# Kernel optimization log

Hardware: AMD Instinct MI355X
Metric: run time of the kernel (lower is better)

## Reference

```python
import jax, jax.numpy as jnp
import numpy as np


def _three_nn(parent_xyz, xyz):
    # parent_xyz: (bs, n, 3) queries; xyz: (bs, m, 3) reference points.
    # Squared pairwise distances (bs, n, m) without forming (x-y)^2 tensor of rank 4.
    d2 = (jnp.sum(parent_xyz**2, -1, keepdims=True)
          - 2.0 * jnp.einsum('bnd,bmd->bnm', parent_xyz, xyz)
          + jnp.sum(xyz**2, -1)[:, None, :])
    neg_d2, idx = jax.lax.top_k(-d2, 3)           # 3 smallest distances
    dist = jnp.sqrt(jnp.maximum(-neg_d2, 0.0))    # pointnet2 returns sqrt(dist2)
    return dist, idx                              # (bs, n, 3), (bs, n, 3)


def _three_interpolate(feats, idx, weight):
    # feats: (bs, c, m); idx, weight: (bs, n, 3) -> (bs, c, n)
    feats_t = jnp.swapaxes(feats, 1, 2)                     # (bs, m, c)
    gathered = jax.vmap(lambda f, i: f[i])(feats_t, idx)    # (bs, n, 3, c)
    out = jnp.einsum('bnkc,bnk->bcn', gathered, weight)
    return out


def _conv1x1(x, W, b):
    # x: (bs, c_in, n); W: (c_out, c_in); b: (c_out,)
    return jnp.einsum('oc,bcn->bon', W, x) + b[None, :, None]


def setup_inputs() -> dict:
    key = jax.random.key(0)
    ks = jax.random.split(key, 6)
    bs, m, n = 8, 1024, 4096
    c0, c1, c2 = 256, 128, 256
    xyz = jax.random.normal(ks[0], (bs, m, 3), jnp.float32)
    parent_xyz = jax.random.normal(ks[1], (bs, n, 3), jnp.float32)
    feats = jax.random.normal(ks[2], (bs, c0, m), jnp.float32)
    skip_feats = jax.random.normal(ks[3], (bs, c1, n), jnp.float32)
    W1 = jax.random.normal(ks[4], (c2, c0 + c1), jnp.float32) * (1.0 / np.sqrt(c0 + c1))
    b1 = jnp.zeros((c2,), jnp.float32)
    W2 = jax.random.normal(ks[5], (c2, c2), jnp.float32) * (1.0 / np.sqrt(c2))
    b2 = jnp.zeros((c2,), jnp.float32)
    return {"xyz": xyz, "parent_xyz": parent_xyz, "feats": feats,
            "skip_feats": skip_feats, "W1": W1, "b1": b1, "W2": W2, "b2": b2}


def reference(xyz, parent_xyz, feats, skip_feats, W1, b1, W2, b2):
    dist, idx = _three_nn(parent_xyz, xyz)
    inv_dist = 1.0 / (dist + 1e-8)
    weight = inv_dist / jnp.sum(inv_dist, 2, keepdims=True)     # (bs, n, 3)
    up_feats = _three_interpolate(feats, idx, weight)           # (bs, c0, n)
    parent_feats = jnp.concatenate([up_feats, skip_feats], 1)   # (bs, c0+c1, n)
    h = jax.nn.relu(_conv1x1(parent_feats, W1, b1))
    out = jax.nn.relu(_conv1x1(h, W2, b2))
    return out
```

## Files before the change

kernel.cpp:

```cpp
#include <hip/hip_runtime.h>
#include <hip/hip_bf16.h>
#include <cstddef>
#include <cstdint>

#define BS    8
#define M_PTS 1024
#define N_PTS 4096
#define C0    256
#define C1    128
#define C2    256
#define K1DIM 384

typedef __attribute__((ext_vector_type(8))) short bf16x8;
typedef __attribute__((ext_vector_type(4))) float f32x4;

__device__ __forceinline__ ushort f2bf(float f) {
  union { float f; unsigned u; } v; v.f = f;
  unsigned r = v.u + 0x7fffu + ((v.u >> 16) & 1u);
  return (ushort)(r >> 16);
}
__device__ __forceinline__ ushort bf16c(float f) {
  return __builtin_bit_cast(ushort, __float2bfloat16(f));
}

__device__ __forceinline__ float rdlane_f(float v, int lane) {
  union { float f; int i; } u; u.f = v;
  u.i = __builtin_amdgcn_readlane(u.i, lane);
  return u.f;
}

__global__ __launch_bounds__(256) void prep_k(
    const float* __restrict__ feats, const float* __restrict__ W1,
    const float* __restrict__ W2, float* __restrict__ featsT,
    ushort* __restrict__ W1f, ushort* __restrict__ W2f) {
  __shared__ float tile[32][33];
  const int t = threadIdx.x;
  if (blockIdx.x < 2048) {
    const int bx = blockIdx.x & 31;
    const int by = (blockIdx.x >> 5) & 7;
    const int bz = blockIdx.x >> 8;
    const int tx = t & 31, ty = t >> 5;
    const float* ip = feats + (size_t)bz * C0 * M_PTS;
    float*       op = featsT + (size_t)bz * C0 * M_PTS;
    const int r0 = by * 32, c0 = bx * 32;
#pragma unroll
    for (int i = 0; i < 4; ++i)
      tile[ty + i * 8][tx] = ip[(size_t)(r0 + ty + i * 8) * M_PTS + c0 + tx];
    __syncthreads();
#pragma unroll
    for (int i = 0; i < 4; ++i)
      op[(size_t)(c0 + ty + i * 8) * C0 + r0 + tx] = tile[tx][ty + i * 8];
  } else {
    const int id = (blockIdx.x - 2048) * 256 + t;
    if (id < C2 * K1DIM) {
      int m = id / K1DIM, k = id - m * K1DIM;
      int off = (((m >> 4) * 12 + (k >> 5)) * 4 + ((k >> 3) & 3)) * 128 + (m & 15) * 8 + (k & 7);
      W1f[off] = f2bf(W1[id]);
    }
    if (id < C2 * C2) {
      int m = id >> 8, k = id & 255;
      int off = (((m >> 4) * 8 + (k >> 5)) * 4 + ((k >> 3) & 3)) * 128 + (m & 15) * 8 + (k & 7);
      W2f[off] = f2bf(W2[id]);
    }
  }
}

__global__ __launch_bounds__(256, 4) void fp_fused_k(
    const float* __restrict__ xyz,
    const float* __restrict__ pxyz,
    const float* __restrict__ featsT,
    const float* __restrict__ skip,
    const ushort* __restrict__ W1f,
    const float* __restrict__ b1,
    const ushort* __restrict__ W2f,
    const float* __restrict__ b2,
    float* __restrict__ out) {
  __shared__ float4 smemq[2560];
  float4* pts4 = smemq;
  ushort* pfB  = (ushort*)(smemq + 1024);
  ushort* hbuf = (ushort*)smemq;

  const int t  = threadIdx.x;
  const int b  = blockIdx.x & 7;
  const int n0 = (blockIdx.x >> 3) * 32;
  const int wv = t >> 6, l = t & 63;
  const int q  = t >> 3, sub = t & 7;

  const float qx = pxyz[((size_t)b * N_PTS + n0 + q) * 3 + 0];
  const float qy = pxyz[((size_t)b * N_PTS + n0 + q) * 3 + 1];
  const float qz = pxyz[((size_t)b * N_PTS + n0 + q) * 3 + 2];

#pragma unroll
  for (int it = 0; it < 2; ++it) {
    const int p = t + it * 256;
    const float2* xb = (const float2*)(xyz + (size_t)b * 3 * M_PTS + 6 * p);
    const float2 A = xb[0], B = xb[1], C = xb[2];
    const float x0 = A.x, y0 = A.y, z0 = B.x, x1 = B.y, y1 = C.x, z1 = C.y;
    const float s0 = __fadd_rn(__fadd_rn(__fmul_rn(x0, x0), __fmul_rn(y0, y0)),
                               __fmul_rn(z0, z0));
    const float s1 = __fadd_rn(__fadd_rn(__fmul_rn(x1, x1), __fmul_rn(y1, y1)),
                               __fmul_rn(z1, z1));
    const int U = p ^ ((p >> 6) & 7);
    pts4[U * 2 + 0] = (float4){x0 + x0, x1 + x1, y0 + y0, y1 + y1};
    pts4[U * 2 + 1] = (float4){z0 + z0, z1 + z1, s0, s1};
  }

  float skp[16];
#pragma unroll
  for (int it = 0; it < 8; ++it) {
    const int id = t + it * 256;
    const int r2 = id >> 5, nn = id & 31;
    skp[2 * it + 0] = skip[((size_t)b * C1 + 2 * r2 + 0) * N_PTS + n0 + nn];
    skp[2 * it + 1] = skip[((size_t)b * C1 + 2 * r2 + 1) * N_PTS + n0 + nn];
  }

  const float qq = __fadd_rn(__fadd_rn(__fmul_rn(qx, qx), __fmul_rn(qy, qy)),
                             __fmul_rn(qz, qz));
  __syncthreads();

  float d0 = 3.4e38f, d1 = 3.4e38f, d2 = 3.4e38f;
  int   i0 = 0, i1 = 0, i2 = 0;
  {
    int pe[8];
#pragma unroll
    for (int e = 0; e < 8; ++e) pe[e] = (sub * 64 + (e ^ sub)) * 2;
    for (int jb = 0; jb < 8; ++jb) {
#pragma unroll
      for (int e = 0; e < 8; ++e) {
        const float4 A  = pts4[pe[e] + jb * 16];
        const float4 Bv = pts4[pe[e] + jb * 16 + 1];
        {
          const float dot2 = __fadd_rn(__fadd_rn(__fmul_rn(qx, A.x), __fmul_rn(qy, A.z)),
                                       __fmul_rn(qz, Bv.x));
          const float d = __fadd_rn(__fsub_rn(qq, dot2), Bv.z);
          const int m = jb * 16 + 2 * e;
          const bool c0 = d < d0, c1 = d < d1, c2 = d < d2;
          i2 = c1 ? i1 : (c2 ? m : i2);
          i1 = c0 ? i0 : (c1 ? m : i1);
          i0 = c0 ? m : i0;
          d2 = __builtin_amdgcn_fmed3f(d, d1, d2);
          d1 = __builtin_amdgcn_fmed3f(d, d0, d1);
          d0 = fminf(d, d0);
        }
        {
          const float dot2 = __fadd_rn(__fadd_rn(__fmul_rn(qx, A.y), __fmul_rn(qy, A.w)),
                                       __fmul_rn(qz, Bv.y));
          const float d = __fadd_rn(__fsub_rn(qq, dot2), Bv.w);
          const int m = jb * 16 + 2 * e + 1;
          const bool c0 = d < d0, c1 = d < d1, c2 = d < d2;
          i2 = c1 ? i1 : (c2 ? m : i2);
          i1 = c0 ? i0 : (c1 ? m : i1);
          i0 = c0 ? m : i0;
          d2 = __builtin_amdgcn_fmed3f(d, d1, d2);
          d1 = __builtin_amdgcn_fmed3f(d, d0, d1);
          d0 = fminf(d, d0);
        }
      }
    }
    i0 += sub * 128; i1 += sub * 128; i2 += sub * 128;
  }

#pragma unroll
  for (int mk = 1; mk <= 4; mk <<= 1) {
    const float pd0 = __shfl_xor(d0, mk), pd1 = __shfl_xor(d1, mk), pd2 = __shfl_xor(d2, mk);
    const int   pi0 = __shfl_xor(i0, mk), pi1 = __shfl_xor(i1, mk), pi2 = __shfl_xor(i2, mk);
    const bool lo = (sub & mk) == 0;
    const float a0 = lo ? d0 : pd0, a1 = lo ? d1 : pd1, a2 = lo ? d2 : pd2;
    const float b0 = lo ? pd0 : d0, b1v = lo ? pd1 : d1, b2v = lo ? pd2 : d2;
    const int   A0 = lo ? i0 : pi0, A1 = lo ? i1 : pi1, A2 = lo ? i2 : pi2;
    const int   B0 = lo ? pi0 : i0, B1 = lo ? pi1 : i1, B2 = lo ? pi2 : i2;
    const bool c0 = b0 < a0;
    const bool cb1a0 = b1v < a0, cb0a1 = b0 < a1;
    const bool cb1a1 = b1v < a1, cb2a0 = b2v < a0, cb0a2 = b0 < a2;
    const float m0 = c0 ? b0 : a0;                 const int M0 = c0 ? B0 : A0;
    const float t1a = cb1a0 ? b1v : a0;            const int T1a = cb1a0 ? B1 : A0;
    const float t1b = cb0a1 ? b0 : a1;             const int T1b = cb0a1 ? B0 : A1;
    const float m1 = c0 ? t1a : t1b;               const int M1 = c0 ? T1a : T1b;
    const float sA = cb2a0 ? b2v : a0;             const int SA = cb2a0 ? B2 : A0;
    const float sB = cb1a1 ? b1v : a1;             const int SB = cb1a1 ? B1 : A1;
    const float sD = cb0a2 ? b0 : a2;              const int SD = cb0a2 ? B0 : A2;
    const float m2 = c0 ? (cb1a0 ? sA : sB) : (cb0a1 ? sB : sD);
    const int   M2 = c0 ? (cb1a0 ? SA : SB) : (cb0a1 ? SB : SD);
    d0 = m0; d1 = m1; d2 = m2; i0 = M0; i1 = M1; i2 = M2;
  }

  float w0f, w1f, w2f;
  {
    const float t0 = sqrtf(fmaxf(d0, 0.f)), t1 = sqrtf(fmaxf(d1, 0.f)),
                t2 = sqrtf(fmaxf(d2, 0.f));
    const float r0 = 1.0f / (t0 + 1e-8f), r1 = 1.0f / (t1 + 1e-8f),
                r2 = 1.0f / (t2 + 1e-8f);
    const float rs = __fadd_rn(__fadd_rn(r0, r1), r2);
    w0f = r0 / rs; w1f = r1 / rs; w2f = r2 / rs;
  }

  {
    const float* fb = featsT + (size_t)b * M_PTS * C0;
    float cw0 = rdlane_f(w0f, 0), cw1 = rdlane_f(w1f, 0), cw2 = rdlane_f(w2f, 0);
    float4 cf0 = *(const float4*)(fb + (size_t)__builtin_amdgcn_readlane(i0, 0) * C0 + l * 4);
    float4 cf1 = *(const float4*)(fb + (size_t)__builtin_amdgcn_readlane(i1, 0) * C0 + l * 4);
    float4 cf2 = *(const float4*)(fb + (size_t)__builtin_amdgcn_readlane(i2, 0) * C0 + l * 4);
#pragma unroll
    for (int qi = 0; qi < 8; ++qi) {
      float nw0, nw1, nw2; float4 nf0, nf1, nf2;
      if (qi < 7) {
        const int src = (qi + 1) * 8;
        nw0 = rdlane_f(w0f, src); nw1 = rdlane_f(w1f, src); nw2 = rdlane_f(w2f, src);
        nf0 = *(const float4*)(fb + (size_t)__builtin_amdgcn_readlane(i0, src) * C0 + l * 4);
        nf1 = *(const float4*)(fb + (size_t)__builtin_amdgcn_readlane(i1, src) * C0 + l * 4);
        nf2 = *(const float4*)(fb + (size_t)__builtin_amdgcn_readlane(i2, src) * C0 + l * 4);
      }
      ushort4 hv;
      hv.x = bf16c(cw0 * cf0.x + cw1 * cf1.x + cw2 * cf2.x);
      hv.y = bf16c(cw0 * cf0.y + cw1 * cf1.y + cw2 * cf2.y);
      hv.z = bf16c(cw0 * cf0.z + cw1 * cf1.z + cw2 * cf2.z);
      hv.w = bf16c(cw0 * cf0.w + cw1 * cf1.w + cw2 * cf2.w);
      const int nq = wv * 8 + qi;
      const int kq = l >> 1;
      const int u = kq * 32 + (nq ^ (kq & 7));
      *reinterpret_cast<ushort4*>(&pfB[u * 8 + (l & 1) * 4]) = hv;
      if (qi < 7) { cf0 = nf0; cf1 = nf1; cf2 = nf2; cw0 = nw0; cw1 = nw1; cw2 = nw2; }
    }
  }
#pragma unroll
  for (int it = 0; it < 8; ++it) {
    const int id = t + it * 256;
    const int r2 = id >> 5, nn = id & 31;
    const int k = C0 + 2 * r2;
    const int kq = k >> 3;
    const int u = kq * 32 + (nn ^ (kq & 7));
    ushort2 sv; sv.x = bf16c(skp[2 * it]); sv.y = bf16c(skp[2 * it + 1]);
    *reinterpret_cast<ushort2*>(&pfB[u * 8 + (k & 7)]) = sv;
  }
  __syncthreads();

  const int c = l & 15, g = l >> 4;

  f32x4 acc[4][2];
#pragma unroll
  for (int i = 0; i < 4; ++i)
#pragma unroll
    for (int j = 0; j < 2; ++j) acc[i][j] = (f32x4){0.f, 0.f, 0.f, 0.f};

  {
    bf16x8 afr[4], nafr[4];
#pragma unroll
    for (int i = 0; i < 4; ++i)
      afr[i] = *reinterpret_cast<const bf16x8*>(&W1f[(((wv * 4 + i) * 12 + 0) * 4 + g) * 128 + c * 8]);
    for (int kb = 0; kb < 12; ++kb) {
      const int kqg = kb * 4 + g;
      bf16x8 bfr[2];
#pragma unroll
      for (int j = 0; j < 2; ++j)
        bfr[j] = *reinterpret_cast<const bf16x8*>(&pfB[(kqg * 32 + ((j * 16 + c) ^ (kqg & 7))) * 8]);
      if (kb < 11) {
#pragma unroll
        for (int i = 0; i < 4; ++i)
          nafr[i] = *reinterpret_cast<const bf16x8*>(&W1f[(((wv * 4 + i) * 12 + kb + 1) * 4 + g) * 128 + c * 8]);
      }
      __builtin_amdgcn_s_setprio(1);
#pragma unroll
      for (int i = 0; i < 4; ++i)
#pragma unroll
        for (int j = 0; j < 2; ++j)
          acc[i][j] = __builtin_amdgcn_mfma_f32_16x16x32_bf16(afr[i], bfr[j], acc[i][j], 0, 0, 0);
      __builtin_amdgcn_s_setprio(0);
      if (kb < 11) {
#pragma unroll
        for (int i = 0; i < 4; ++i) afr[i] = nafr[i];
      }
    }
  }

#pragma unroll
  for (int i = 0; i < 4; ++i) {
    const int mbase = wv * 64 + i * 16 + g * 4;
    const float4 bias = *(const float4*)(b1 + mbase);
#pragma unroll
    for (int j = 0; j < 2; ++j) {
      const int nn = j * 16 + c;
      const int kq = mbase >> 3;
      const int u = kq * 32 + (nn ^ (kq & 7));
      ushort4 hv;
      hv.x = bf16c(fmaxf(acc[i][j].x + bias.x, 0.f));
      hv.y = bf16c(fmaxf(acc[i][j].y + bias.y, 0.f));
      hv.z = bf16c(fmaxf(acc[i][j].z + bias.z, 0.f));
      hv.w = bf16c(fmaxf(acc[i][j].w + bias.w, 0.f));
      *reinterpret_cast<ushort4*>(&hbuf[u * 8 + (mbase & 7)]) = hv;
    }
  }
  __syncthreads();

#pragma unroll
  for (int i = 0; i < 4; ++i)
#pragma unroll
    for (int j = 0; j < 2; ++j) acc[i][j] = (f32x4){0.f, 0.f, 0.f, 0.f};

  {
    bf16x8 afr[4], nafr[4];
#pragma unroll
    for (int i = 0; i < 4; ++i)
      afr[i] = *reinterpret_cast<const bf16x8*>(&W2f[(((wv * 4 + i) * 8 + 0) * 4 + g) * 128 + c * 8]);
    for (int kb = 0; kb < 8; ++kb) {
      const int kqg = kb * 4 + g;
      bf16x8 bfr[2];
#pragma unroll
      for (int j = 0; j < 2; ++j)
        bfr[j] = *reinterpret_cast<const bf16x8*>(&hbuf[(kqg * 32 + ((j * 16 + c) ^ (kqg & 7))) * 8]);
      if (kb < 7) {
#pragma unroll
        for (int i = 0; i < 4; ++i)
          nafr[i] = *reinterpret_cast<const bf16x8*>(&W2f[(((wv * 4 + i) * 8 + kb + 1) * 4 + g) * 128 + c * 8]);
      }
      __builtin_amdgcn_s_setprio(1);
#pragma unroll
      for (int i = 0; i < 4; ++i)
#pragma unroll
        for (int j = 0; j < 2; ++j)
          acc[i][j] = __builtin_amdgcn_mfma_f32_16x16x32_bf16(afr[i], bfr[j], acc[i][j], 0, 0, 0);
      __builtin_amdgcn_s_setprio(0);
      if (kb < 7) {
#pragma unroll
        for (int i = 0; i < 4; ++i) afr[i] = nafr[i];
      }
    }
  }

#pragma unroll
  for (int i = 0; i < 4; ++i) {
    const int mbase = wv * 64 + i * 16 + g * 4;
    const float4 bias = *(const float4*)(b2 + mbase);
#pragma unroll
    for (int j = 0; j < 2; ++j) {
      const int nn = n0 + j * 16 + c;
      out[((size_t)b * C2 + mbase + 0) * N_PTS + nn] = fmaxf(acc[i][j].x + bias.x, 0.f);
      out[((size_t)b * C2 + mbase + 1) * N_PTS + nn] = fmaxf(acc[i][j].y + bias.y, 0.f);
      out[((size_t)b * C2 + mbase + 2) * N_PTS + nn] = fmaxf(acc[i][j].z + bias.z, 0.f);
      out[((size_t)b * C2 + mbase + 3) * N_PTS + nn] = fmaxf(acc[i][j].w + bias.w, 0.f);
    }
  }
}

extern "C" void kernel_launch(void* const* d_in, const int* in_sizes, int n_in,
                              void* d_out, int out_size, void* d_ws, size_t ws_size,
                              hipStream_t stream) {
  const float* xyz   = (const float*)d_in[0];
  const float* pxyz  = (const float*)d_in[1];
  const float* feats = (const float*)d_in[2];
  const float* skip  = (const float*)d_in[3];
  const float* W1    = (const float*)d_in[4];
  const float* b1    = (const float*)d_in[5];
  const float* W2    = (const float*)d_in[6];
  const float* b2    = (const float*)d_in[7];
  float* out = (float*)d_out;

  float*  ws     = (float*)d_ws;
  float*  featsT = ws;
  ushort* W1f    = (ushort*)(featsT + (size_t)BS * M_PTS * C0);
  ushort* W2f    = W1f + (size_t)C2 * K1DIM;

  prep_k<<<2432, 256, 0, stream>>>(feats, W1, W2, featsT, W1f, W2f);
  fp_fused_k<<<BS * (N_PTS / 32), 256, 0, stream>>>(xyz, pxyz, featsT, skip,
                                                    W1f, b1, W2f, b2, out);
}
```

Measured before the change: 45.55 us.

## Precompute W1·feats at coarse points and interpolate projected features

Uses linearity of the interpolation and the first 1x1 conv: the prep kernel now computes G = W1[:, :C0]·feats at the m coarse points with MFMA and stores it transposed. The fused kernel then interpolates G rows straight into the accumulators. The first GEMM shrinks to only the skip-feature K range (128 instead of 384), and the per-query gather of 256-channel feature rows is replaced by gathers of 256-wide projected rows. This trades a feats transpose for a small extra GEMM over m=1024 points. It also changes rounding, since the interpolation now runs in fp32 on bf16-projected results instead of bf16-rounding the interpolated features.

```diff
diff --git a/kernel.cpp b/kernel.cpp
--- a/kernel.cpp
+++ b/kernel.cpp
@@ -23,35 +23,13 @@
   return __builtin_bit_cast(ushort, __float2bfloat16(f));
 }
 
-__device__ __forceinline__ float rdlane_f(float v, int lane) {
-  union { float f; int i; } u; u.f = v;
-  u.i = __builtin_amdgcn_readlane(u.i, lane);
-  return u.f;
-}
-
 __global__ __launch_bounds__(256) void prep_k(
     const float* __restrict__ feats, const float* __restrict__ W1,
-    const float* __restrict__ W2, float* __restrict__ featsT,
-    ushort* __restrict__ W1f, ushort* __restrict__ W2f) {
-  __shared__ float tile[32][33];
+    const float* __restrict__ W2, ushort* __restrict__ W1f,
+    ushort* __restrict__ W2f, float* __restrict__ Gt) {
   const int t = threadIdx.x;
-  if (blockIdx.x < 2048) {
-    const int bx = blockIdx.x & 31;
-    const int by = (blockIdx.x >> 5) & 7;
-    const int bz = blockIdx.x >> 8;
-    const int tx = t & 31, ty = t >> 5;
-    const float* ip = feats + (size_t)bz * C0 * M_PTS;
-    float*       op = featsT + (size_t)bz * C0 * M_PTS;
-    const int r0 = by * 32, c0 = bx * 32;
-#pragma unroll
-    for (int i = 0; i < 4; ++i)
-      tile[ty + i * 8][tx] = ip[(size_t)(r0 + ty + i * 8) * M_PTS + c0 + tx];
-    __syncthreads();
-#pragma unroll
-    for (int i = 0; i < 4; ++i)
-      op[(size_t)(c0 + ty + i * 8) * C0 + r0 + tx] = tile[tx][ty + i * 8];
-  } else {
-    const int id = (blockIdx.x - 2048) * 256 + t;
+  if (blockIdx.x < 384) {
+    const int id = blockIdx.x * 256 + t;
     if (id < C2 * K1DIM) {
       int m = id / K1DIM, k = id - m * K1DIM;
       int off = (((m >> 4) * 12 + (k >> 5)) * 4 + ((k >> 3) & 3)) * 128 + (m & 15) * 8 + (k & 7);
@@ -62,23 +40,84 @@
       int off = (((m >> 4) * 8 + (k >> 5)) * 4 + ((k >> 3) & 3)) * 128 + (m & 15) * 8 + (k & 7);
       W2f[off] = f2bf(W2[id]);
     }
-  }
+    return;
+  }
+  __shared__ ushort Bt[16384];
+  const int id2 = blockIdx.x - 384;
+  const int bz = id2 & 7;
+  const int m0 = (id2 >> 3) * 64;
+  const float* fb = feats + (size_t)bz * C0 * M_PTS;
+
+#pragma unroll
+  for (int it = 0; it < 16; ++it) {
+    const int cc = it * 16 + (t >> 4);
+    const int nl = (t & 15) * 4;
+    const float4 v = *(const float4*)(fb + (size_t)cc * M_PTS + m0 + nl);
+    const int kq = cc >> 3, ko = cc & 7;
+    Bt[(kq * 64 + ((nl + 0) ^ (kq & 7))) * 8 + ko] = bf16c(v.x);
+    Bt[(kq * 64 + ((nl + 1) ^ (kq & 7))) * 8 + ko] = bf16c(v.y);
+    Bt[(kq * 64 + ((nl + 2) ^ (kq & 7))) * 8 + ko] = bf16c(v.z);
+    Bt[(kq * 64 + ((nl + 3) ^ (kq & 7))) * 8 + ko] = bf16c(v.w);
+  }
+  __syncthreads();
+
+  const int wv = t >> 6, l = t & 63, c = l & 15, g = l >> 4;
+  f32x4 acc[4][4];
+#pragma unroll
+  for (int i = 0; i < 4; ++i)
+#pragma unroll
+    for (int j = 0; j < 4; ++j) acc[i][j] = (f32x4){0.f, 0.f, 0.f, 0.f};
+
+  for (int kb = 0; kb < 8; ++kb) {
+    const int kqg = kb * 4 + g;
+    bf16x8 bfr[4], afr[4];
+#pragma unroll
+    for (int j = 0; j < 4; ++j)
+      bfr[j] = *reinterpret_cast<const bf16x8*>(&Bt[(kqg * 64 + ((j * 16 + c) ^ (kqg & 7))) * 8]);
+#pragma unroll
+    for (int i = 0; i < 4; ++i) {
+      const float* wr = W1 + (size_t)((wv * 4 + i) * 16 + c) * K1DIM + kb * 32 + g * 8;
+      const float4 a0 = *(const float4*)wr;
+      const float4 a1 = *(const float4*)(wr + 4);
+      bf16x8 af;
+      af[0] = (short)bf16c(a0.x); af[1] = (short)bf16c(a0.y);
+      af[2] = (short)bf16c(a0.z); af[3] = (short)bf16c(a0.w);
+      af[4] = (short)bf16c(a1.x); af[5] = (short)bf16c(a1.y);
+      af[6] = (short)bf16c(a1.z); af[7] = (short)bf16c(a1.w);
+      afr[i] = af;
+    }
+#pragma unroll
+    for (int i = 0; i < 4; ++i)
+#pragma unroll
+      for (int j = 0; j < 4; ++j)
+        acc[i][j] = __builtin_amdgcn_mfma_f32_16x16x32_bf16(afr[i], bfr[j], acc[i][j], 0, 0, 0);
+  }
+
+  float* gtb = Gt + (size_t)bz * M_PTS * C2;
+#pragma unroll
+  for (int i = 0; i < 4; ++i)
+#pragma unroll
+    for (int j = 0; j < 4; ++j)
+      *reinterpret_cast<float4*>(gtb + (size_t)(m0 + j * 16 + c) * C2 + (wv * 4 + i) * 16 + g * 4)
+          = *reinterpret_cast<float4*>(&acc[i][j]);
 }
 
 __global__ __launch_bounds__(256, 4) void fp_fused_k(
     const float* __restrict__ xyz,
     const float* __restrict__ pxyz,
-    const float* __restrict__ featsT,
+    const float* __restrict__ Gt,
     const float* __restrict__ skip,
     const ushort* __restrict__ W1f,
     const float* __restrict__ b1,
     const ushort* __restrict__ W2f,
     const float* __restrict__ b2,
     float* __restrict__ out) {
-  __shared__ float4 smemq[2560];
-  float4* pts4 = smemq;
-  ushort* pfB  = (ushort*)(smemq + 1024);
-  ushort* hbuf = (ushort*)smemq;
+  __shared__ float4 smemq[1584];
+  float4* pts4  = smemq;
+  ushort* pfB   = (ushort*)smemq + 8192;
+  int*    idx_s = (int*)((char*)smemq + 24576);
+  float*  w_s   = (float*)((char*)smemq + 24960);
+  ushort* hbuf  = (ushort*)smemq;
 
   const int t  = threadIdx.x;
   const int b  = blockIdx.x & 7;
@@ -105,13 +144,16 @@
     pts4[U * 2 + 1] = (float4){z0 + z0, z1 + z1, s0, s1};
   }
 
-  float skp[16];
 #pragma unroll
   for (int it = 0; it < 8; ++it) {
     const int id = t + it * 256;
     const int r2 = id >> 5, nn = id & 31;
-    skp[2 * it + 0] = skip[((size_t)b * C1 + 2 * r2 + 0) * N_PTS + n0 + nn];
-    skp[2 * it + 1] = skip[((size_t)b * C1 + 2 * r2 + 1) * N_PTS + n0 + nn];
+    const float s0v = skip[((size_t)b * C1 + 2 * r2 + 0) * N_PTS + n0 + nn];
+    const float s1v = skip[((size_t)b * C1 + 2 * r2 + 1) * N_PTS + n0 + nn];
+    const int kl = 2 * r2;
+    const int kq = kl >> 3;
+    ushort2 sv; sv.x = bf16c(s0v); sv.y = bf16c(s1v);
+    *reinterpret_cast<ushort2*>(&pfB[(kq * 32 + (nn ^ (kq & 7))) * 8 + (kl & 7)]) = sv;
   }
 
   const float qq = __fadd_rn(__fadd_rn(__fmul_rn(qx, qx), __fmul_rn(qy, qy)),
@@ -184,92 +226,64 @@
     d0 = m0; d1 = m1; d2 = m2; i0 = M0; i1 = M1; i2 = M2;
   }
 
-  float w0f, w1f, w2f;
-  {
+  if (sub == 0) {
     const float t0 = sqrtf(fmaxf(d0, 0.f)), t1 = sqrtf(fmaxf(d1, 0.f)),
                 t2 = sqrtf(fmaxf(d2, 0.f));
     const float r0 = 1.0f / (t0 + 1e-8f), r1 = 1.0f / (t1 + 1e-8f),
                 r2 = 1.0f / (t2 + 1e-8f);
     const float rs = __fadd_rn(__fadd_rn(r0, r1), r2);
-    w0f = r0 / rs; w1f = r1 / rs; w2f = r2 / rs;
-  }
+    idx_s[q * 3 + 0] = i0; idx_s[q * 3 + 1] = i1; idx_s[q * 3 + 2] = i2;
+    w_s[q * 3 + 0] = r0 / rs; w_s[q * 3 + 1] = r1 / rs; w_s[q * 3 + 2] = r2 / rs;
+  }
+  __syncthreads();
+
+  const int c = l & 15, g = l >> 4;
+
+  f32x4 acc[4][2];
+#pragma unroll
+  for (int i = 0; i < 4; ++i)
+#pragma unroll
+    for (int j = 0; j < 2; ++j) acc[i][j] = (f32x4){0.f, 0.f, 0.f, 0.f};
 
   {
-    const float* fb = featsT + (size_t)b * M_PTS * C0;
-    float cw0 = rdlane_f(w0f, 0), cw1 = rdlane_f(w1f, 0), cw2 = rdlane_f(w2f, 0);
-    float4 cf0 = *(const float4*)(fb + (size_t)__builtin_amdgcn_readlane(i0, 0) * C0 + l * 4);
-    float4 cf1 = *(const float4*)(fb + (size_t)__builtin_amdgcn_readlane(i1, 0) * C0 + l * 4);
-    float4 cf2 = *(const float4*)(fb + (size_t)__builtin_amdgcn_readlane(i2, 0) * C0 + l * 4);
-#pragma unroll
-    for (int qi = 0; qi < 8; ++qi) {
-      float nw0, nw1, nw2; float4 nf0, nf1, nf2;
-      if (qi < 7) {
-        const int src = (qi + 1) * 8;
-        nw0 = rdlane_f(w0f, src); nw1 = rdlane_f(w1f, src); nw2 = rdlane_f(w2f, src);
-        nf0 = *(const float4*)(fb + (size_t)__builtin_amdgcn_readlane(i0, src) * C0 + l * 4);
-        nf1 = *(const float4*)(fb + (size_t)__builtin_amdgcn_readlane(i1, src) * C0 + l * 4);
-        nf2 = *(const float4*)(fb + (size_t)__builtin_amdgcn_readlane(i2, src) * C0 + l * 4);
+    const float* gtb = Gt + (size_t)b * M_PTS * C2;
+#pragma unroll
+    for (int j = 0; j < 2; ++j) {
+      const int nq = j * 16 + c;
+      const int j0 = idx_s[nq * 3 + 0], j1 = idx_s[nq * 3 + 1], j2 = idx_s[nq * 3 + 2];
+      const float w0 = w_s[nq * 3 + 0], w1 = w_s[nq * 3 + 1], w2 = w_s[nq * 3 + 2];
+      const float* g0p = gtb + (size_t)j0 * C2 + wv * 64 + g * 4;
+      const float* g1p = gtb + (size_t)j1 * C2 + wv * 64 + g * 4;
+      const float* g2p = gtb + (size_t)j2 * C2 + wv * 64 + g * 4;
+#pragma unroll
+      for (int i = 0; i < 4; ++i) {
+        const float4 f0 = *(const float4*)(g0p + i * 16);
+        const float4 f1 = *(const float4*)(g1p + i * 16);
+        const float4 f2 = *(const float4*)(g2p + i * 16);
+        acc[i][j].x += w0 * f0.x + w1 * f1.x + w2 * f2.x;
+        acc[i][j].y += w0 * f0.y + w1 * f1.y + w2 * f2.y;
+        acc[i][j].z += w0 * f0.z + w1 * f1.z + w2 * f2.z;
+        acc[i][j].w += w0 * f0.w + w1 * f1.w + w2 * f2.w;
       }
-      ushort4 hv;
-      hv.x = bf16c(cw0 * cf0.x + cw1 * cf1.x + cw2 * cf2.x);
-      hv.y = bf16c(cw0 * cf0.y + cw1 * cf1.y + cw2 * cf2.y);
-      hv.z = bf16c(cw0 * cf0.z + cw1 * cf1.z + cw2 * cf2.z);
-      hv.w = bf16c(cw0 * cf0.w + cw1 * cf1.w + cw2 * cf2.w);
-      const int nq = wv * 8 + qi;
-      const int kq = l >> 1;
-      const int u = kq * 32 + (nq ^ (kq & 7));
-      *reinterpret_cast<ushort4*>(&pfB[u * 8 + (l & 1) * 4]) = hv;
-      if (qi < 7) { cf0 = nf0; cf1 = nf1; cf2 = nf2; cw0 = nw0; cw1 = nw1; cw2 = nw2; }
-    }
-  }
-#pragma unroll
-  for (int it = 0; it < 8; ++it) {
-    const int id = t + it * 256;
-    const int r2 = id >> 5, nn = id & 31;
-    const int k = C0 + 2 * r2;
-    const int kq = k >> 3;
-    const int u = kq * 32 + (nn ^ (kq & 7));
-    ushort2 sv; sv.x = bf16c(skp[2 * it]); sv.y = bf16c(skp[2 * it + 1]);
-    *reinterpret_cast<ushort2*>(&pfB[u * 8 + (k & 7)]) = sv;
-  }
-  __syncthreads();
-
-  const int c = l & 15, g = l >> 4;
-
-  f32x4 acc[4][2];
-#pragma unroll
-  for (int i = 0; i < 4; ++i)
-#pragma unroll
-    for (int j = 0; j < 2; ++j) acc[i][j] = (f32x4){0.f, 0.f, 0.f, 0.f};
-
-  {
-    bf16x8 afr[4], nafr[4];
+    }
+  }
+
+  for (int kb = 0; kb < 4; ++kb) {
+    const int kqg = kb * 4 + g;
+    bf16x8 bfr[2], afr[4];
+#pragma unroll
+    for (int j = 0; j < 2; ++j)
+      bfr[j] = *reinterpret_cast<const bf16x8*>(&pfB[(kqg * 32 + ((j * 16 + c) ^ (kqg & 7))) * 8]);
 #pragma unroll
     for (int i = 0; i < 4; ++i)
-      afr[i] = *reinterpret_cast<const bf16x8*>(&W1f[(((wv * 4 + i) * 12 + 0) * 4 + g) * 128 + c * 8]);
-    for (int kb = 0; kb < 12; ++kb) {
-      const int kqg = kb * 4 + g;
-      bf16x8 bfr[2];
+      afr[i] = *reinterpret_cast<const bf16x8*>(&W1f[(((wv * 4 + i) * 12 + kb + 8) * 4 + g) * 128 + c * 8]);
+    __builtin_amdgcn_s_setprio(1);
+#pragma unroll
+    for (int i = 0; i < 4; ++i)
 #pragma unroll
       for (int j = 0; j < 2; ++j)
-        bfr[j] = *reinterpret_cast<const bf16x8*>(&pfB[(kqg * 32 + ((j * 16 + c) ^ (kqg & 7))) * 8]);
-      if (kb < 11) {
-#pragma unroll
-        for (int i = 0; i < 4; ++i)
-          nafr[i] = *reinterpret_cast<const bf16x8*>(&W1f[(((wv * 4 + i) * 12 + kb + 1) * 4 + g) * 128 + c * 8]);
-      }
-      __builtin_amdgcn_s_setprio(1);
-#pragma unroll
-      for (int i = 0; i < 4; ++i)
-#pragma unroll
-        for (int j = 0; j < 2; ++j)
-          acc[i][j] = __builtin_amdgcn_mfma_f32_16x16x32_bf16(afr[i], bfr[j], acc[i][j], 0, 0, 0);
-      __builtin_amdgcn_s_setprio(0);
-      if (kb < 11) {
-#pragma unroll
-        for (int i = 0; i < 4; ++i) afr[i] = nafr[i];
-      }
-    }
+        acc[i][j] = __builtin_amdgcn_mfma_f32_16x16x32_bf16(afr[i], bfr[j], acc[i][j], 0, 0, 0);
+    __builtin_amdgcn_s_setprio(0);
   }
 
 #pragma unroll
@@ -354,12 +368,11 @@
   const float* b2    = (const float*)d_in[7];
   float* out = (float*)d_out;
 
-  float*  ws     = (float*)d_ws;
-  float*  featsT = ws;
-  ushort* W1f    = (ushort*)(featsT + (size_t)BS * M_PTS * C0);
-  ushort* W2f    = W1f + (size_t)C2 * K1DIM;
-
-  prep_k<<<2432, 256, 0, stream>>>(feats, W1, W2, featsT, W1f, W2f);
-  fp_fused_k<<<BS * (N_PTS / 32), 256, 0, stream>>>(xyz, pxyz, featsT, skip,
+  ushort* W1f = (ushort*)d_ws;
+  ushort* W2f = W1f + (size_t)C2 * K1DIM;
+  float*  Gt  = (float*)(W2f + (size_t)C2 * C2);
+
+  prep_k<<<512, 256, 0, stream>>>(feats, W1, W2, W1f, W2f, Gt);
+  fp_fused_k<<<BS * (N_PTS / 32), 256, 0, stream>>>(xyz, pxyz, Gt, skip,
                                                     W1f, b1, W2f, b2, out);
 }
```

After: 52.48 us. 15.2% more time.

## Split first GEMM K-loop into two halves to shrink LDS and raise occupancy

Applied to the files above, without the earlier changes.

The concatenated activation tile in shared memory is now staged in two halves: the first 192 K-rows (lanes below 48 of the gather) are computed, consumed by the first six MFMA K-blocks, then overwritten by the remaining gathered features plus skip features for the last six K-blocks. This cuts the shared buffer from 2560 to 1792 float4 and raises the launch-bounds occupancy hint from 4 to 5 blocks. The software prefetch of the next gather row and next W1 fragment is removed. In exchange it adds two extra block barriers and serialises gather and MFMA phases, with less latency hiding per wave.

```diff
diff --git a/kernel.cpp b/kernel.cpp
--- a/kernel.cpp
+++ b/kernel.cpp
@@ -22,7 +22,6 @@
 __device__ __forceinline__ ushort bf16c(float f) {
   return __builtin_bit_cast(ushort, __float2bfloat16(f));
 }
-
 __device__ __forceinline__ float rdlane_f(float v, int lane) {
   union { float f; int i; } u; u.f = v;
   u.i = __builtin_amdgcn_readlane(u.i, lane);
@@ -65,7 +64,7 @@
   }
 }
 
-__global__ __launch_bounds__(256, 4) void fp_fused_k(
+__global__ __launch_bounds__(256, 5) void fp_fused_k(
     const float* __restrict__ xyz,
     const float* __restrict__ pxyz,
     const float* __restrict__ featsT,
@@ -75,9 +74,9 @@
     const ushort* __restrict__ W2f,
     const float* __restrict__ b2,
     float* __restrict__ out) {
-  __shared__ float4 smemq[2560];
+  __shared__ float4 smemq[1792];
   float4* pts4 = smemq;
-  ushort* pfB  = (ushort*)(smemq + 1024);
+  ushort* pfBh = (ushort*)smemq + 8192;
   ushort* hbuf = (ushort*)smemq;
 
   const int t  = threadIdx.x;
@@ -194,82 +193,109 @@
     w0f = r0 / rs; w1f = r1 / rs; w2f = r2 / rs;
   }
 
-  {
-    const float* fb = featsT + (size_t)b * M_PTS * C0;
-    float cw0 = rdlane_f(w0f, 0), cw1 = rdlane_f(w1f, 0), cw2 = rdlane_f(w2f, 0);
-    float4 cf0 = *(const float4*)(fb + (size_t)__builtin_amdgcn_readlane(i0, 0) * C0 + l * 4);
-    float4 cf1 = *(const float4*)(fb + (size_t)__builtin_amdgcn_readlane(i1, 0) * C0 + l * 4);
-    float4 cf2 = *(const float4*)(fb + (size_t)__builtin_amdgcn_readlane(i2, 0) * C0 + l * 4);
+  const float* fb = featsT + (size_t)b * M_PTS * C0;
+
+  if (l < 48) {
 #pragma unroll
     for (int qi = 0; qi < 8; ++qi) {
-      float nw0, nw1, nw2; float4 nf0, nf1, nf2;
-      if (qi < 7) {
-        const int src = (qi + 1) * 8;
-        nw0 = rdlane_f(w0f, src); nw1 = rdlane_f(w1f, src); nw2 = rdlane_f(w2f, src);
-        nf0 = *(const float4*)(fb + (size_t)__builtin_amdgcn_readlane(i0, src) * C0 + l * 4);
-        nf1 = *(const float4*)(fb + (size_t)__builtin_amdgcn_readlane(i1, src) * C0 + l * 4);
-        nf2 = *(const float4*)(fb + (size_t)__builtin_amdgcn_readlane(i2, src) * C0 + l * 4);
-      }
+      const int src = qi * 8;
+      const int  j0 = __builtin_amdgcn_readlane(i0, src);
+      const int  j1 = __builtin_amdgcn_readlane(i1, src);
+      const int  j2 = __builtin_amdgcn_readlane(i2, src);
+      const float w0 = rdlane_f(w0f, src), w1 = rdlane_f(w1f, src), w2 = rdlane_f(w2f, src);
+      const float4 f0 = *(const float4*)(fb + (size_t)j0 * C0 + l * 4);
+      const float4 f1 = *(const float4*)(fb + (size_t)j1 * C0 + l * 4);
+      const float4 f2 = *(const float4*)(fb + (size_t)j2 * C0 + l * 4);
       ushort4 hv;
-      hv.x = bf16c(cw0 * cf0.x + cw1 * cf1.x + cw2 * cf2.x);
-      hv.y = bf16c(cw0 * cf0.y + cw1 * cf1.y + cw2 * cf2.y);
-      hv.z = bf16c(cw0 * cf0.z + cw1 * cf1.z + cw2 * cf2.z);
-      hv.w = bf16c(cw0 * cf0.w + cw1 * cf1.w + cw2 * cf2.w);
+      hv.x = bf16c(w0 * f0.x + w1 * f1.x + w2 * f2.x);
+      hv.y = bf16c(w0 * f0.y + w1 * f1.y + w2 * f2.y);
+      hv.z = bf16c(w0 * f0.z + w1 * f1.z + w2 * f2.z);
+      hv.w = bf16c(w0 * f0.w + w1 * f1.w + w2 * f2.w);
       const int nq = wv * 8 + qi;
       const int kq = l >> 1;
       const int u = kq * 32 + (nq ^ (kq & 7));
-      *reinterpret_cast<ushort4*>(&pfB[u * 8 + (l & 1) * 4]) = hv;
-      if (qi < 7) { cf0 = nf0; cf1 = nf1; cf2 = nf2; cw0 = nw0; cw1 = nw1; cw2 = nw2; }
+      *reinterpret_cast<ushort4*>(&pfBh[u * 8 + (l & 1) * 4]) = hv;
+    }
+  }
+  __syncthreads();
+
+  const int c = l & 15, g = l >> 4;
+
+  f32x4 acc[4][2];
+#pragma unroll
+  for (int i = 0; i < 4; ++i)
+#pragma unroll
+    for (int j = 0; j < 2; ++j) acc[i][j] = (f32x4){0.f, 0.f, 0.f, 0.f};
+
+  for (int kb = 0; kb < 6; ++kb) {
+    const int kqg = kb * 4 + g;
+    bf16x8 bfr[2], afr[4];
+#pragma unroll
+    for (int j = 0; j < 2; ++j)
+      bfr[j] = *reinterpret_cast<const bf16x8*>(&pfBh[(kqg * 32 + ((j * 16 + c) ^ (kqg & 7))) * 8]);
+#pragma unroll
+    for (int i = 0; i < 4; ++i)
+      afr[i] = *reinterpret_cast<const bf16x8*>(&W1f[(((wv * 4 + i) * 12 + kb) * 4 + g) * 128 + c * 8]);
+    __builtin_amdgcn_s_setprio(1);
+#pragma unroll
+    for (int i = 0; i < 4; ++i)
+#pragma unroll
+      for (int j = 0; j < 2; ++j)
+        acc[i][j] = __builtin_amdgcn_mfma_f32_16x16x32_bf16(afr[i], bfr[j], acc[i][j], 0, 0, 0);
+    __builtin_amdgcn_s_setprio(0);
+  }
+  __syncthreads();
+
+  if (l >= 48) {
+#pragma unroll
+    for (int qi = 0; qi < 8; ++qi) {
+      const int src = qi * 8;
+      const int  j0 = __builtin_amdgcn_readlane(i0, src);
+      const int  j1 = __builtin_amdgcn_readlane(i1, src);
+      const int  j2 = __builtin_amdgcn_readlane(i2, src);
+      const float w0 = rdlane_f(w0f, src), w1 = rdlane_f(w1f, src), w2 = rdlane_f(w2f, src);
+      const float4 f0 = *(const float4*)(fb + (size_t)j0 * C0 + l * 4);
+      const float4 f1 = *(const float4*)(fb + (size_t)j1 * C0 + l * 4);
+      const float4 f2 = *(const float4*)(fb + (size_t)j2 * C0 + l * 4);
+      ushort4 hv;
+      hv.x = bf16c(w0 * f0.x + w1 * f1.x + w2 * f2.x);
+      hv.y = bf16c(w0 * f0.y + w1 * f1.y + w2 * f2.y);
+      hv.z = bf16c(w0 * f0.z + w1 * f1.z + w2 * f2.z);
+      hv.w = bf16c(w0 * f0.w + w1 * f1.w + w2 * f2.w);
+      const int nq = wv * 8 + qi;
+      const int kq = (l - 48) >> 1;
+      const int u = kq * 32 + (nq ^ (kq & 7));
+      *reinterpret_cast<ushort4*>(&pfBh[u * 8 + (l & 1) * 4]) = hv;
     }
   }
 #pragma unroll
   for (int it = 0; it < 8; ++it) {
     const int id = t + it * 256;
     const int r2 = id >> 5, nn = id & 31;
-    const int k = C0 + 2 * r2;
-    const int kq = k >> 3;
+    const int kl = 64 + 2 * r2;
+    const int kq = kl >> 3;
     const int u = kq * 32 + (nn ^ (kq & 7));
     ushort2 sv; sv.x = bf16c(skp[2 * it]); sv.y = bf16c(skp[2 * it + 1]);
-    *reinterpret_cast<ushort2*>(&pfB[u * 8 + (k & 7)]) = sv;
-  }
-  __syncthreads();
-
-  const int c = l & 15, g = l >> 4;
-
-  f32x4 acc[4][2];
-#pragma unroll
-  for (int i = 0; i < 4; ++i)
-#pragma unroll
-    for (int j = 0; j < 2; ++j) acc[i][j] = (f32x4){0.f, 0.f, 0.f, 0.f};
-
-  {
-    bf16x8 afr[4], nafr[4];
-#pragma unroll
-    for (int i = 0; i < 4; ++i)
-      afr[i] = *reinterpret_cast<const bf16x8*>(&W1f[(((wv * 4 + i) * 12 + 0) * 4 + g) * 128 + c * 8]);
-    for (int kb = 0; kb < 12; ++kb) {
-      const int kqg = kb * 4 + g;
-      bf16x8 bfr[2];
+    *reinterpret_cast<ushort2*>(&pfBh[u * 8 + (kl & 7)]) = sv;
+  }
+  __syncthreads();
+
+  for (int kb = 6; kb < 12; ++kb) {
+    const int kql = (kb - 6) * 4 + g;
+    bf16x8 bfr[2], afr[4];
+#pragma unroll
+    for (int j = 0; j < 2; ++j)
+      bfr[j] = *reinterpret_cast<const bf16x8*>(&pfBh[(kql * 32 + ((j * 16 + c) ^ (kql & 7))) * 8]);
+#pragma unroll
+    for (int i = 0; i < 4; ++i)
+      afr[i] = *reinterpret_cast<const bf16x8*>(&W1f[(((wv * 4 + i) * 12 + kb) * 4 + g) * 128 + c * 8]);
+    __builtin_amdgcn_s_setprio(1);
+#pragma unroll
+    for (int i = 0; i < 4; ++i)
 #pragma unroll
       for (int j = 0; j < 2; ++j)
-        bfr[j] = *reinterpret_cast<const bf16x8*>(&pfB[(kqg * 32 + ((j * 16 + c) ^ (kqg & 7))) * 8]);
-      if (kb < 11) {
-#pragma unroll
-        for (int i = 0; i < 4; ++i)
-          nafr[i] = *reinterpret_cast<const bf16x8*>(&W1f[(((wv * 4 + i) * 12 + kb + 1) * 4 + g) * 128 + c * 8]);
-      }
-      __builtin_amdgcn_s_setprio(1);
-#pragma unroll
-      for (int i = 0; i < 4; ++i)
-#pragma unroll
-        for (int j = 0; j < 2; ++j)
-          acc[i][j] = __builtin_amdgcn_mfma_f32_16x16x32_bf16(afr[i], bfr[j], acc[i][j], 0, 0, 0);
-      __builtin_amdgcn_s_setprio(0);
-      if (kb < 11) {
-#pragma unroll
-        for (int i = 0; i < 4; ++i) afr[i] = nafr[i];
-      }
-    }
+        acc[i][j] = __builtin_amdgcn_mfma_f32_16x16x32_bf16(afr[i], bfr[j], acc[i][j], 0, 0, 0);
+    __builtin_amdgcn_s_setprio(0);
   }
 
 #pragma unroll
```

Result: slower. 57.42 us (+26.0%).
